# Kernel optimization log

Hardware: AMD Instinct MI355X
Metric: run time of the kernel (lower is better)

## Reference

```python
import jax, jax.numpy as jnp
import numpy as np


def setup_inputs() -> dict:
    key = jax.random.key(0)
    B, A, C, H, W = 16, 3, 80, 76, 76
    output = jax.random.normal(key, (B, (C + 5) * A, H, W), dtype=jnp.float32)
    # anchors are divided by stride in the module's __init__ (stride=8)
    anchors = jnp.array([[10.0, 13.0], [16.0, 30.0], [33.0, 23.0]], dtype=jnp.float32) / 8.0
    return {"output": output, "anchors": anchors}


def reference(output, anchors):
    # Dense YOLO grid decode (get_region_boxes without the data-dependent
    # threshold extraction, which just filters these values on CPU).
    B, c, H, W = output.shape
    A = anchors.shape[0]
    C = c // A - 5
    out = output.reshape(B, A, C + 5, H, W)  # anchor-major channel groups
    anchors = jax.lax.stop_gradient(anchors)  # matches Aw.detach()/Ah.detach()

    gx = jnp.arange(W, dtype=output.dtype)            # [W], broadcast over H
    gy = jnp.arange(H, dtype=output.dtype)[:, None]   # [H,1]
    aw = anchors[:, 0][None, :, None, None]           # [1,A,1,1]
    ah = anchors[:, 1][None, :, None, None]

    xs = (jax.nn.sigmoid(out[:, :, 0]) + gx) / W      # [B,A,H,W] normalized cx
    ys = (jax.nn.sigmoid(out[:, :, 1]) + gy) / H
    ws = (jnp.exp(out[:, :, 2]) * aw) / W
    hs = (jnp.exp(out[:, :, 3]) * ah) / H
    conf = jax.nn.sigmoid(out[:, :, 4])

    cls_logits = out[:, :, 5:]                        # [B,A,C,H,W]
    cls_conf = jax.lax.stop_gradient(jax.nn.softmax(cls_logits, axis=2))  # .detach()
    cls_prob = jnp.max(cls_conf, axis=2)              # [B,A,H,W]
    cls_id = jax.lax.stop_gradient(
        jnp.argmax(cls_conf, axis=2).astype(output.dtype))

    # [B,A,H,W,7]: cx, cy, w, h, box_conf, cls_prob, cls_id (as float)
    boxes = jnp.stack([xs, ys, ws, hs, conf, cls_prob, cls_id], axis=-1)
    return boxes
```

## Files before the change

kernel.cpp:

```cpp
#include <hip/hip_runtime.h>


#define B_  16
#define A_  3
#define C_  80
#define H_  76
#define W_  76
#define PLANE (H_ * W_)

__device__ __forceinline__ float fast_exp(float x) {
    return __builtin_amdgcn_exp2f(x * 1.44269504088896340736f);
}

__device__ __forceinline__ float fast_rcp(float x) {
    return __builtin_amdgcn_rcpf(x);
}

__device__ __forceinline__ float sigmoidf(float x) {
    return fast_rcp(1.0f + fast_exp(-x));
}

__global__ __launch_bounds__(256) void yolo_kernel(const float* __restrict__ in,
                                                   const float* __restrict__ anchors,
                                                   float* __restrict__ out) {
    const int pos = blockIdx.x * 256 + threadIdx.x;
    if (pos >= PLANE) return;
    const int a = blockIdx.y;
    const int b = blockIdx.z;

    const int x = pos % W_;
    const int y = pos / W_;

    const float* base = in + (size_t)(b * (A_ * (C_ + 5)) + a * (C_ + 5)) * PLANE + pos;

    float t[5];
    #pragma unroll
    for (int c = 0; c < 5; ++c) t[c] = base[c * PLANE];

    float l[C_];
    #pragma unroll
    for (int c = 0; c < C_; ++c) l[c] = base[(size_t)(5 + c) * PLANE];

    const float aw = anchors[2 * a + 0];
    const float ah = anchors[2 * a + 1];

    const float xs   = (sigmoidf(t[0]) + (float)x) * (1.0f / (float)W_);
    const float ys   = (sigmoidf(t[1]) + (float)y) * (1.0f / (float)H_);
    const float ws   = fast_exp(t[2]) * aw * (1.0f / (float)W_);
    const float hs   = fast_exp(t[3]) * ah * (1.0f / (float)H_);
    const float conf = sigmoidf(t[4]);

    float m = l[0];
    int   id = 0;
    #pragma unroll
    for (int c = 1; c < C_; ++c) {
        if (l[c] > m) { m = l[c]; id = c; }
    }
    float s = 0.0f;
    #pragma unroll
    for (int c = 0; c < C_; ++c) s += fast_exp(l[c] - m);

    const float cls_prob = fast_rcp(s);
    const float cls_id   = (float)id;

    const size_t o = (size_t)((b * A_ + a) * PLANE + pos) * 7;
    out[o + 0] = xs;
    out[o + 1] = ys;
    out[o + 2] = ws;
    out[o + 3] = hs;
    out[o + 4] = conf;
    out[o + 5] = cls_prob;
    out[o + 6] = cls_id;
}

extern "C" void kernel_launch(void* const* d_in, const int* in_sizes, int n_in,
                              void* d_out, int out_size, void* d_ws, size_t ws_size,
                              hipStream_t stream) {
    const float* in      = (const float*)d_in[0];
    const float* anchors = (const float*)d_in[1];
    float* out           = (float*)d_out;

    dim3 grid((PLANE + 255) / 256, A_, B_);
    dim3 block(256, 1, 1);
    yolo_kernel<<<grid, block, 0, stream>>>(in, anchors, out);
}
```

Before: 139.9 us.

## Split class reduction across four waves per position and stage output through LDS

```diff
diff --git a/kernel.cpp b/kernel.cpp
--- a/kernel.cpp
+++ b/kernel.cpp
@@ -7,6 +7,7 @@
 #define H_  76
 #define W_  76
 #define PLANE (H_ * W_)
+#define CPW  20
 
 __device__ __forceinline__ float fast_exp(float x) {
     return __builtin_amdgcn_exp2f(x * 1.44269504088896340736f);
@@ -23,54 +24,86 @@
 __global__ __launch_bounds__(256) void yolo_kernel(const float* __restrict__ in,
                                                    const float* __restrict__ anchors,
                                                    float* __restrict__ out) {
-    const int pos = blockIdx.x * 256 + threadIdx.x;
-    if (pos >= PLANE) return;
+    const int tid  = threadIdx.x;
+    const int lane = tid & 63;
+    const int wid  = tid >> 6;
     const int a = blockIdx.y;
     const int b = blockIdx.z;
+    const int pos_base = blockIdx.x * 64;
+    const int pos  = pos_base + lane;
+    const int posc = (pos < PLANE) ? pos : (PLANE - 1);
 
-    const int x = pos % W_;
-    const int y = pos / W_;
+    const float* base = in + (size_t)((b * A_ + a) * (C_ + 5)) * PLANE + posc;
 
-    const float* base = in + (size_t)(b * (A_ * (C_ + 5)) + a * (C_ + 5)) * PLANE + pos;
+    const float* cb = base + (size_t)(5 + wid * CPW) * PLANE;
+    float l[CPW];
+    #pragma unroll
+    for (int j = 0; j < CPW; ++j) l[j] = cb[(size_t)j * PLANE];
 
-    float t[5];
-    #pragma unroll
-    for (int c = 0; c < 5; ++c) t[c] = base[c * PLANE];
-
-    float l[C_];
-    #pragma unroll
-    for (int c = 0; c < C_; ++c) l[c] = base[(size_t)(5 + c) * PLANE];
-
-    const float aw = anchors[2 * a + 0];
-    const float ah = anchors[2 * a + 1];
-
-    const float xs   = (sigmoidf(t[0]) + (float)x) * (1.0f / (float)W_);
-    const float ys   = (sigmoidf(t[1]) + (float)y) * (1.0f / (float)H_);
-    const float ws   = fast_exp(t[2]) * aw * (1.0f / (float)W_);
-    const float hs   = fast_exp(t[3]) * ah * (1.0f / (float)H_);
-    const float conf = sigmoidf(t[4]);
+    float t0 = 0.f, t1 = 0.f, t2 = 0.f, t3 = 0.f, t4 = 0.f;
+    if (wid == 0) {
+        t0 = base[0 * PLANE];
+        t1 = base[1 * PLANE];
+        t2 = base[2 * PLANE];
+        t3 = base[3 * PLANE];
+        t4 = base[4 * PLANE];
+    }
 
     float m = l[0];
     int   id = 0;
     #pragma unroll
-    for (int c = 1; c < C_; ++c) {
-        if (l[c] > m) { m = l[c]; id = c; }
+    for (int j = 1; j < CPW; ++j) {
+        if (l[j] > m) { m = l[j]; id = j; }
     }
     float s = 0.0f;
     #pragma unroll
-    for (int c = 0; c < C_; ++c) s += fast_exp(l[c] - m);
+    for (int j = 0; j < CPW; ++j) s += fast_exp(l[j] - m);
 
-    const float cls_prob = fast_rcp(s);
-    const float cls_id   = (float)id;
+    __shared__ float sm[4][64];
+    __shared__ float ss[4][64];
+    __shared__ int   sid[4][64];
+    __shared__ float res[64 * 7];
 
-    const size_t o = (size_t)((b * A_ + a) * PLANE + pos) * 7;
-    out[o + 0] = xs;
-    out[o + 1] = ys;
-    out[o + 2] = ws;
-    out[o + 3] = hs;
-    out[o + 4] = conf;
-    out[o + 5] = cls_prob;
-    out[o + 6] = cls_id;
+    sm[wid][lane]  = m;
+    ss[wid][lane]  = s;
+    sid[wid][lane] = id + wid * CPW;
+    __syncthreads();
+
+    if (wid == 0) {
+        float M  = sm[0][lane];
+        int   ID = sid[0][lane];
+        #pragma unroll
+        for (int w = 1; w < 4; ++w) {
+            const float mw = sm[w][lane];
+            if (mw > M) { M = mw; ID = sid[w][lane]; }
+        }
+        float S = 0.0f;
+        #pragma unroll
+        for (int w = 0; w < 4; ++w) S += ss[w][lane] * fast_exp(sm[w][lane] - M);
+
+        const int x = posc % W_;
+        const int y = posc / W_;
+        const float aw = anchors[2 * a + 0];
+        const float ah = anchors[2 * a + 1];
+
+        res[lane * 7 + 0] = (sigmoidf(t0) + (float)x) * (1.0f / (float)W_);
+        res[lane * 7 + 1] = (sigmoidf(t1) + (float)y) * (1.0f / (float)H_);
+        res[lane * 7 + 2] = fast_exp(t2) * aw * (1.0f / (float)W_);
+        res[lane * 7 + 3] = fast_exp(t3) * ah * (1.0f / (float)H_);
+        res[lane * 7 + 4] = sigmoidf(t4);
+        res[lane * 7 + 5] = fast_rcp(S);
+        res[lane * 7 + 6] = (float)ID;
+    }
+    __syncthreads();
+
+    const size_t obase = (size_t)((b * A_ + a) * PLANE + pos_base) * 7;
+    #pragma unroll
+    for (int k = 0; k < 2; ++k) {
+        const int f = tid + k * 256;
+        if (f < 64 * 7 && (pos_base + f / 7) < PLANE) {
+            out[obase + f] = res[f];
+        }
+    }
 }
 
 extern "C" void kernel_launch(void* const* d_in, const int* in_sizes, int n_in,
@@ -80,7 +113,7 @@
     const float* anchors = (const float*)d_in[1];
     float* out           = (float*)d_out;
 
-    dim3 grid((PLANE + 255) / 256, A_, B_);
+    dim3 grid((PLANE + 63) / 64, A_, B_);
     dim3 block(256, 1, 1);
     yolo_kernel<<<grid, block, 0, stream>>>(in, anchors, out);
 }
```

Measured after the change: 136.6 us. 2.4% less time.
